# Kernel tuning notes

Measured on AMD Instinct MI355X. Metric: run time of the kernel, lower is better.

The kernel has to match this reference:

```python
import jax, jax.numpy as jnp
import numpy as np

B, P, C = 4, 2048, 1024
N_HEADS = 16
HEAD = C // N_HEADS


def setup_inputs() -> dict:
    key = jax.random.key(0)
    ks = jax.random.split(key, 9)
    s = C ** -0.5
    return {
        "x": jax.random.normal(ks[0], (B, P, C), dtype=jnp.float32),
        "Wq": jax.random.normal(ks[1], (C, C), dtype=jnp.float32) * s,
        "bq": jnp.zeros((C,), dtype=jnp.float32),
        "Wk": jax.random.normal(ks[2], (C, C), dtype=jnp.float32) * s,
        "bk": jnp.zeros((C,), dtype=jnp.float32),
        "Wv": jax.random.normal(ks[3], (C, C), dtype=jnp.float32) * s,
        "bv": jnp.zeros((C,), dtype=jnp.float32),
        "Wo": jax.random.normal(ks[4], (C, C), dtype=jnp.float32) * s,
        "bo": jnp.zeros((C,), dtype=jnp.float32),
    }


def _attn(x, Wq, bq, Wk, bk, Wv, bv, Wo, bo):
    b, p, c = x.shape
    q = (x @ Wq + bq).reshape(b, p, N_HEADS, HEAD).transpose(0, 2, 1, 3)
    k = (x @ Wk + bk).reshape(b, p, N_HEADS, HEAD).transpose(0, 2, 1, 3)
    v = (x @ Wv + bv).reshape(b, p, N_HEADS, HEAD).transpose(0, 2, 1, 3)
    # scores: [B, H, P, P]
    w = jnp.einsum('bhqd,bhkd->bhqk', q, k) * (HEAD ** -0.5)
    w = jax.nn.softmax(w, axis=-1)
    y = jnp.einsum('bhqk,bhkd->bhqd', w, v)
    y = y.transpose(0, 2, 1, 3).reshape(b, p, c)
    return y @ Wo + bo


def reference(x, Wq, bq, Wk, bk, Wv, bv, Wo, bo):
    return _attn(x, Wq, bq, Wk, bk, Wv, bv, Wo, bo)
```

## Files before the change

kernel.cpp:

```cpp
#include <hip/hip_runtime.h>

#define B_DIM 4
#define P_DIM 2048
#define C_DIM 1024
#define H_CNT 16
#define D_HEAD 64
#define M_DIM 8192
#define K_DIM 1024

typedef __attribute__((ext_vector_type(4))) float  f32x4;
typedef __attribute__((ext_vector_type(8))) __bf16 bf16x8;
typedef __attribute__((ext_vector_type(4))) __bf16 bf16x4;
typedef __attribute__((ext_vector_type(4))) short  s16x4;
typedef __attribute__((ext_vector_type(8))) short  s16x8;

static __device__ __forceinline__ short f2bf(float f) {
    unsigned u = __float_as_uint(f);
    u += 0x7fff + ((u >> 16) & 1);
    return (short)(u >> 16);
}

#define GLDS16(src, dst) __builtin_amdgcn_global_load_lds( \
    (__attribute__((address_space(1))) void*)(void*)(src), \
    (__attribute__((address_space(3))) void*)(void*)(dst), 16, 0, 0)

__global__ __launch_bounds__(256) void cvt_f32_bf16(const float* __restrict__ in,
                                                    short* __restrict__ out) {
    size_t i = ((size_t)blockIdx.x * 256 + threadIdx.x) * 4;
    f32x4 v = *(const f32x4*)(in + i);
    s16x4 o;
    o[0] = f2bf(v[0]); o[1] = f2bf(v[1]); o[2] = f2bf(v[2]); o[3] = f2bf(v[3]);
    *(s16x4*)(out + i) = o;
}

__global__ __launch_bounds__(256) void wtrans_all(const float* __restrict__ W0,
                                                  const float* __restrict__ W1,
                                                  const float* __restrict__ W2,
                                                  const float* __restrict__ W3,
                                                  short* __restrict__ WT) {
    __shared__ float t[32][33];
    const int z = blockIdx.z;
    const float* W = z == 0 ? W0 : z == 1 ? W1 : z == 2 ? W2 : W3;
    short* dst = WT + (size_t)z * C_DIM * C_DIM;
    const int k0 = blockIdx.y * 32, n0 = blockIdx.x * 32;
    const int tx = threadIdx.x & 31, ty = threadIdx.x >> 5;
#pragma unroll
    for (int j = 0; j < 4; ++j)
        t[ty + j * 8][tx] = W[(size_t)(k0 + ty + j * 8) * C_DIM + n0 + tx];
    __syncthreads();
#pragma unroll
    for (int j = 0; j < 4; ++j)
        dst[(size_t)(n0 + ty + j * 8) * C_DIM + k0 + tx] = f2bf(t[tx][ty + j * 8]);
}

template<int MODE>
__global__ __launch_bounds__(256) void gemm_bt(const short* __restrict__ A,
                                               const short* __restrict__ BT,
                                               const float* __restrict__ bias,
                                               const float* __restrict__ bias2,
                                               void* __restrict__ outp,
                                               int gx) {
    const int h = blockIdx.y * gx + blockIdx.x;
    const int cpx = (gx << 6) >> 3;
    const int lid = (h & 7) * cpx + (h >> 3);
    const int m0 = (lid / gx) * 128;
    const int n0 = (lid % gx) * 128;

    __shared__ __align__(16) short lA[128 * 32];
    __shared__ __align__(16) short lB[128 * 32];
    const int tid = threadIdx.x;
    const int lane = tid & 63;
    const int w = tid >> 6;
    const int wr = (w >> 1) * 64;
    const int wc = (w & 1) * 64;
    const int li = lane & 15, g = lane >> 4;

    f32x4 acc[4][4] = {};

    const int r0s = tid >> 2, r1s = (tid + 256) >> 2;
    const int c0 = (tid & 3) ^ ((r0s >> 1) & 3);
    const int c1 = (tid & 3) ^ ((r1s >> 1) & 3);
    const short* a0 = A + (size_t)(m0 + r0s) * K_DIM + c0 * 8;
    const short* a1 = A + (size_t)(m0 + r1s) * K_DIM + c1 * 8;
    const short* b0 = BT + (size_t)(n0 + r0s) * K_DIM + c0 * 8;
    const short* b1 = BT + (size_t)(n0 + r1s) * K_DIM + c1 * 8;
    short* lA0 = lA + w * 512;  short* lA1 = lA + 2048 + w * 512;
    short* lB0 = lB + w * 512;  short* lB1 = lB + 2048 + w * 512;

    int aoff[4], boff[4];
#pragma unroll
    for (int i = 0; i < 4; ++i) {
        int ra = wr + i * 16 + li;  int pa = g ^ ((ra >> 1) & 3);
        aoff[i] = ra * 32 + pa * 8;
        int rb = wc + i * 16 + li;  int pb = g ^ ((rb >> 1) & 3);
        boff[i] = rb * 32 + pb * 8;
    }

    for (int k0 = 0; k0 < K_DIM; k0 += 32) {
        __syncthreads();
        GLDS16(a0 + k0, lA0);
        GLDS16(a1 + k0, lA1);
        GLDS16(b0 + k0, lB0);
        GLDS16(b1 + k0, lB1);
        __syncthreads();
        bf16x8 af[4], bfr[4];
#pragma unroll
        for (int i = 0; i < 4; ++i) {
            af[i]  = *(const bf16x8*)&lA[aoff[i]];
            bfr[i] = *(const bf16x8*)&lB[boff[i]];
        }
#pragma unroll
        for (int i = 0; i < 4; ++i)
#pragma unroll
            for (int j = 0; j < 4; ++j) {
                if (MODE == 2)
                    acc[i][j] = __builtin_amdgcn_mfma_f32_16x16x32_bf16(
                        af[i], bfr[j], acc[i][j], 0, 0, 0);
                else
                    acc[i][j] = __builtin_amdgcn_mfma_f32_16x16x32_bf16(
                        bfr[j], af[i], acc[i][j], 0, 0, 0);
            }
    }

    if (MODE == 0) {
#pragma unroll
        for (int j = 0; j < 4; ++j) {
            const int nb = n0 + wc + j * 16 + 4 * g;
            const float* bp = nb < 1024 ? bias : bias2;
            const float sc = nb < 1024 ? 0.125f : 1.0f;
            const f32x4 bb = *(const f32x4*)&bp[nb & 1023];
            const int hI = (nb >> 6) & 15, d = nb & 63;
            short* base = (short*)outp + (size_t)(nb >> 10) * M_DIM * C_DIM;
#pragma unroll
            for (int i = 0; i < 4; ++i) {
                const int m = m0 + wr + i * 16 + li;
                const int bI = m >> 11, p = m & 2047;
                s16x4 v4;
#pragma unroll
                for (int r = 0; r < 4; ++r) v4[r] = f2bf((acc[i][j][r] + bb[r]) * sc);
                *(s16x4*)&base[(((size_t)bI * H_CNT + hI) * P_DIM + p) * D_HEAD + d] = v4;
            }
        }
    } else if (MODE == 1) {
#pragma unroll
        for (int j = 0; j < 4; ++j) {
            const int nb = n0 + wc + j * 16 + 4 * g;
            const f32x4 bb = *(const f32x4*)&bias[nb];
#pragma unroll
            for (int i = 0; i < 4; ++i) {
                const int m = m0 + wr + i * 16 + li;
                f32x4 v;
#pragma unroll
                for (int r = 0; r < 4; ++r) v[r] = acc[i][j][r] + bb[r];
                *(f32x4*)&((float*)outp)[(size_t)m * C_DIM + nb] = v;
            }
        }
    } else {
#pragma unroll
        for (int j = 0; j < 4; ++j) {
            const int nn = n0 + wc + j * 16 + li;
            const float bb = bias[nn];
            const int hI = nn >> 6, d = nn & 63;
#pragma unroll
            for (int i = 0; i < 4; ++i) {
                const int pbse = m0 + wr + i * 16 + 4 * g;
                const int bI = pbse >> 11, p = pbse & 2047;
                s16x4 v4;
#pragma unroll
                for (int r = 0; r < 4; ++r) v4[r] = f2bf(acc[i][j][r] + bb);
                *(s16x4*)&((short*)outp)[(((size_t)bI * H_CNT + hI) * D_HEAD + d) * P_DIM + p] = v4;
            }
        }
    }
}

__global__ __launch_bounds__(256, 4) void attn_fwd(const short* __restrict__ Q,
                                                   const short* __restrict__ Kb,
                                                   const short* __restrict__ VT,
                                                   short* __restrict__ Y) {
    const int flat = blockIdx.y * 16 + blockIdx.x;
    const int xcd = flat & 7, rr = flat >> 3;
    const int bh = xcd + 8 * (rr >> 4);
    const int qx = rr & 15;

    const int b = bh >> 4, h = bh & 15;
    const int tid = threadIdx.x;
    const int w = tid >> 6, lane = tid & 63;
    const int li = lane & 15, g = lane >> 4;
    const int x7 = li & 7;
    const int q0 = qx * 128 + w * 32;
    const short* Qh = Q + (size_t)bh * P_DIM * D_HEAD;
    const short* Kh = Kb + (size_t)bh * P_DIM * D_HEAD;
    const short* Vh = VT + (size_t)bh * D_HEAD * P_DIM;

    __shared__ __align__(16) short lK[64 * 64];
    __shared__ __align__(16) short lV[64 * 64];
    __shared__ __align__(16) short pb[4][32 * 64];
    short* pw = pb[w];

    bf16x8 qf[2][2];
#pragma unroll
    for (int qt = 0; qt < 2; ++qt)
#pragma unroll
        for (int c = 0; c < 2; ++c)
            qf[qt][c] = *(const bf16x8*)&Qh[(size_t)(q0 + qt * 16 + li) * D_HEAD + c * 32 + g * 8];

    f32x4 o[2][4] = {};
    float ps[2] = {};

    const int t1 = tid + 256;
    const int r0 = tid >> 3, u0 = (tid & 7) ^ (r0 & 7);
    const int r1 = t1 >> 3,  u1 = (t1 & 7) ^ (r1 & 7);
    const short* ks0 = Kh + r0 * D_HEAD + u0 * 8;
    const short* ks1 = Kh + r1 * D_HEAD + u1 * 8;
    const short* vs0 = Vh + r0 * P_DIM + u0 * 8;
    const short* vs1 = Vh + r1 * P_DIM + u1 * 8;
    short* dk0 = lK + tid * 8;  short* dk1 = lK + t1 * 8;
    short* dv0 = lV + tid * 8;  short* dv1 = lV + t1 * 8;

    const int pwrow0 = li * 64;
    const int wsw = x7 << 1;

    for (int k0 = 0; k0 < P_DIM; k0 += 64) {
        __syncthreads();
        GLDS16(ks0 + (size_t)k0 * D_HEAD, dk0);
        GLDS16(ks1 + (size_t)k0 * D_HEAD, dk1);
        GLDS16(vs0 + k0, dv0);
        GLDS16(vs1 + k0, dv1);
        __syncthreads();

        bf16x8 kf[4][2];
#pragma unroll
        for (int kt = 0; kt < 4; ++kt) {
            const int rbase = (kt * 16 + li) * 64;
            kf[kt][0] = *(const bf16x8*)&lK[rbase + ((0 + g) ^ x7) * 8];
            kf[kt][1] = *(const bf16x8*)&lK[rbase + ((4 + g) ^ x7) * 8];
        }

#pragma unroll
        for (int qt = 0; qt < 2; ++qt) {
            f32x4 s[4] = {};
#pragma unroll
            for (int kt = 0; kt < 4; ++kt) {
                s[kt] = __builtin_amdgcn_mfma_f32_16x16x32_bf16(kf[kt][0], qf[qt][0], s[kt], 0, 0, 0);
                s[kt] = __builtin_amdgcn_mfma_f32_16x16x32_bf16(kf[kt][1], qf[qt][1], s[kt], 0, 0, 0);
            }
            const int rowb = pwrow0 + qt * 16 * 64;
#pragma unroll
            for (int kt = 0; kt < 4; ++kt) {
                bf16x4 pv4;
#pragma unroll
                for (int r = 0; r < 4; ++r) {
                    float e = __expf(s[kt][r]);
                    ps[qt] += e;
                    pv4[r] = (__bf16)e;
                }
                const int j = (kt * 4 + g) ^ wsw;
                *(bf16x4*)&pw[rowb + j * 4] = pv4;
            }
        }
        __builtin_amdgcn_sched_barrier(0);
        asm volatile("s_waitcnt lgkmcnt(0)" ::: "memory");
        __builtin_amdgcn_sched_barrier(0);
#pragma unroll
        for (int kc = 0; kc < 2; ++kc) {
            bf16x8 pf[2];
#pragma unroll
            for (int qt = 0; qt < 2; ++qt) {
                const int j = (8 * kc + 2 * g) ^ wsw;
                pf[qt] = *(const bf16x8*)&pw[(qt * 16 + li) * 64 + j * 4];
            }
#pragma unroll
            for (int dt = 0; dt < 4; ++dt) {
                bf16x8 vf = *(const bf16x8*)&lV[(dt * 16 + li) * 64 + ((kc * 4 + g) ^ x7) * 8];
                o[0][dt] = __builtin_amdgcn_mfma_f32_16x16x32_bf16(pf[0], vf, o[0][dt], 0, 0, 0);
                o[1][dt] = __builtin_amdgcn_mfma_f32_16x16x32_bf16(pf[1], vf, o[1][dt], 0, 0, 0);
            }
        }
    }

#pragma unroll
    for (int qt = 0; qt < 2; ++qt) {
        float v = ps[qt];
        v += __shfl_xor(v, 16);
        v += __shfl_xor(v, 32);
#pragma unroll
        for (int r = 0; r < 4; ++r) {
            const float inv = 1.0f / __shfl(v, 4 * g + r);
            const int p = q0 + qt * 16 + 4 * g + r;
            short* yrow = Y + ((size_t)b * P_DIM + p) * C_DIM + h * D_HEAD;
#pragma unroll
            for (int dt = 0; dt < 4; ++dt)
                yrow[dt * 16 + li] = f2bf(o[qt][dt][r] * inv);
        }
    }
}

extern "C" void kernel_launch(void* const* d_in, const int* in_sizes, int n_in,
                              void* d_out, int out_size, void* d_ws, size_t ws_size,
                              hipStream_t stream) {
    (void)in_sizes; (void)n_in; (void)out_size; (void)ws_size;
    const float* x  = (const float*)d_in[0];
    const float* Wq = (const float*)d_in[1];
    const float* bq = (const float*)d_in[2];
    const float* Wk = (const float*)d_in[3];
    const float* bk = (const float*)d_in[4];
    const float* Wv = (const float*)d_in[5];
    const float* bv = (const float*)d_in[6];
    const float* Wo = (const float*)d_in[7];
    const float* bo = (const float*)d_in[8];

    short* ws  = (short*)d_ws;
    short* xb  = ws;
    short* wqt = xb  + (size_t)M_DIM * C_DIM;
    short* wvt = wqt + 2 * (size_t)C_DIM * C_DIM;
    short* wot = wqt + 3 * (size_t)C_DIM * C_DIM;
    short* qd  = wot + (size_t)C_DIM * C_DIM;
    short* kd  = qd  + (size_t)M_DIM * C_DIM;
    short* vtd = kd  + (size_t)M_DIM * C_DIM;
    short* yd  = vtd + (size_t)M_DIM * C_DIM;

    cvt_f32_bf16<<<dim3(M_DIM * C_DIM / 1024), 256, 0, stream>>>(x, xb);
    wtrans_all<<<dim3(32, 32, 4), 256, 0, stream>>>(Wq, Wk, Wv, Wo, wqt);
    gemm_bt<0><<<dim3(16, 64), 256, 0, stream>>>(xb, wqt, bq, bk, (void*)qd, 16);
    gemm_bt<2><<<dim3(8, 64), 256, 0, stream>>>(xb, wvt, bv, nullptr, (void*)vtd, 8);
    attn_fwd<<<dim3(16, 64), 256, 0, stream>>>(qd, kd, vtd, yd);
    gemm_bt<1><<<dim3(8, 64), 256, 0, stream>>>(yd, wot, bo, nullptr, d_out, 8);
}
```

Before: 202.1 us.

## Add dedicated 256x256-tile double-buffered QK projection GEMM kernel

```diff
diff --git a/kernel.cpp b/kernel.cpp
--- a/kernel.cpp
+++ b/kernel.cpp
@@ -51,6 +51,129 @@
 #pragma unroll
     for (int j = 0; j < 4; ++j)
         dst[(size_t)(n0 + ty + j * 8) * C_DIM + k0 + tx] = f2bf(t[tx][ty + j * 8]);
+}
+
+__global__ __launch_bounds__(512, 2) void gemm_qk8(const short* __restrict__ A,
+                                                   const short* __restrict__ BT,
+                                                   const float* __restrict__ bias,
+                                                   const float* __restrict__ bias2,
+                                                   short* __restrict__ outp) {
+    __shared__ __align__(16) short lA[2][256 * 64];
+    __shared__ __align__(16) short lB[2][256 * 64];
+    const int tid = threadIdx.x;
+    const int lane = tid & 63;
+    const int w = tid >> 6;
+    const int wm = w >> 2, wn = w & 3;
+    const int li = lane & 15, g = lane >> 4;
+
+    const int flat = blockIdx.y * 8 + blockIdx.x;
+    const int lid = (flat & 7) * 32 + (flat >> 3);
+    const int m0 = (lid >> 3) * 256;
+    const int n0 = (lid & 7) * 256;
+
+    const int e0 = tid, e1 = tid + 512;
+    const int r0 = e0 >> 3, lu0 = (e0 & 7) ^ (r0 & 7);
+    const int r1 = e1 >> 3, lu1 = (e1 & 7) ^ (r1 & 7);
+    const short* aS0 = A + (size_t)(m0 + r0) * K_DIM + lu0 * 8;
+    const short* aS1 = A + (size_t)(m0 + r1) * K_DIM + lu1 * 8;
+    const short* bS0 = BT + (size_t)(n0 + r0) * K_DIM + lu0 * 8;
+    const short* bS1 = BT + (size_t)(n0 + r1) * K_DIM + lu1 * 8;
+    const int dA0 = e0 * 8, dA1 = e1 * 8;
+
+#define STAGE_A8(buf, hh, kt) do { \
+    GLDS16(aS0 + (size_t)(hh) * 128 * K_DIM + (kt) * 64, &lA[buf][(hh) * 8192 + dA0]); \
+    GLDS16(aS1 + (size_t)(hh) * 128 * K_DIM + (kt) * 64, &lA[buf][(hh) * 8192 + dA1]); } while (0)
+#define STAGE_B8(buf, hh, kt) do { \
+    GLDS16(bS0 + (size_t)(hh) * 128 * K_DIM + (kt) * 64, &lB[buf][(hh) * 8192 + dB0]); \
+    GLDS16(bS1 + (size_t)(hh) * 128 * K_DIM + (kt) * 64, &lB[buf][(hh) * 8192 + dB1]); } while (0)
+    const int dB0 = dA0, dB1 = dA1;
+
+    int aoff[8][2], boff[4][2];
+#pragma unroll
+    for (int mrep = 0; mrep < 8; ++mrep) {
+        const int row = wm * 128 + mrep * 16 + li;
+#pragma unroll
+        for (int ks = 0; ks < 2; ++ks)
+            aoff[mrep][ks] = row * 64 + (((ks * 4 + g) ^ (row & 7)) * 8);
+    }
+#pragma unroll
+    for (int nrep = 0; nrep < 4; ++nrep) {
+        const int row = wn * 64 + nrep * 16 + li;
+#pragma unroll
+        for (int ks = 0; ks < 2; ++ks)
+            boff[nrep][ks] = row * 64 + (((ks * 4 + g) ^ (row & 7)) * 8);
+    }
+
+    f32x4 acc[8][4] = {};
+
+    STAGE_A8(0, 0, 0); STAGE_A8(0, 1, 0);
+    STAGE_B8(0, 0, 0); STAGE_B8(0, 1, 0);
+    asm volatile("s_waitcnt vmcnt(0)" ::: "memory");
+    __builtin_amdgcn_s_barrier();
+
+    for (int t = 0; t < 16; ++t) {
+        const int buf = t & 1;
+        const short* LA = lA[buf];
+        const short* LB = lB[buf];
+        bf16x8 bf[4][2];
+#pragma unroll
+        for (int p = 0; p < 4; ++p) {
+            if (p == 0) {
+#pragma unroll
+                for (int nrep = 0; nrep < 4; ++nrep)
+#pragma unroll
+                    for (int ks = 0; ks < 2; ++ks)
+                        bf[nrep][ks] = *(const bf16x8*)&LB[boff[nrep][ks]];
+            }
+            bf16x8 af2[2][2];
+#pragma unroll
+            for (int i = 0; i < 2; ++i)
+#pragma unroll
+                for (int ks = 0; ks < 2; ++ks)
+                    af2[i][ks] = *(const bf16x8*)&LA[aoff[2 * p + i][ks]];
+            if (t < 15) {
+                if (p == 0)      STAGE_A8(buf ^ 1, 0, t + 1);
+                else if (p == 1) STAGE_A8(buf ^ 1, 1, t + 1);
+                else if (p == 2) STAGE_B8(buf ^ 1, 0, t + 1);
+                else             STAGE_B8(buf ^ 1, 1, t + 1);
+            }
+            __builtin_amdgcn_s_barrier();
+            __builtin_amdgcn_s_setprio(1);
+#pragma unroll
+            for (int ks = 0; ks < 2; ++ks)
+#pragma unroll
+                for (int i = 0; i < 2; ++i)
+#pragma unroll
+                    for (int j = 0; j < 4; ++j)
+                        acc[2 * p + i][j] = __builtin_amdgcn_mfma_f32_16x16x32_bf16(
+                            bf[j][ks], af2[i][ks], acc[2 * p + i][j], 0, 0, 0);
+            __builtin_amdgcn_s_setprio(0);
+            __builtin_amdgcn_s_barrier();
+        }
+        asm volatile("s_waitcnt vmcnt(0)" ::: "memory");
+        __builtin_amdgcn_s_barrier();
+    }
+
+#pragma unroll
+    for (int nrep = 0; nrep < 4; ++nrep) {
+        const int nb = n0 + wn * 64 + nrep * 16 + 4 * g;
+        const float* bp = nb < 1024 ? bias : bias2;
+        const float sc = nb < 1024 ? 0.125f : 1.0f;
+        const f32x4 bb = *(const f32x4*)&bp[nb & 1023];
+        const int hI = (nb >> 6) & 15, d = nb & 63;
+        short* base = outp + (size_t)(nb >> 10) * M_DIM * C_DIM;
+#pragma unroll
+        for (int mrep = 0; mrep < 8; ++mrep) {
+            const int m = m0 + wm * 128 + mrep * 16 + li;
+            const int bI = m >> 11, p = m & 2047;
+            s16x4 v4;
+#pragma unroll
+            for (int r = 0; r < 4; ++r) v4[r] = f2bf((acc[mrep][nrep][r] + bb[r]) * sc);
+            *(s16x4*)&base[(((size_t)bI * H_CNT + hI) * P_DIM + p) * D_HEAD + d] = v4;
+        }
+    }
+#undef STAGE_A8
+#undef STAGE_B8
 }
 
 template<int MODE>
@@ -122,26 +245,7 @@
             }
     }
 
-    if (MODE == 0) {
-#pragma unroll
-        for (int j = 0; j < 4; ++j) {
-            const int nb = n0 + wc + j * 16 + 4 * g;
-            const float* bp = nb < 1024 ? bias : bias2;
-            const float sc = nb < 1024 ? 0.125f : 1.0f;
-            const f32x4 bb = *(const f32x4*)&bp[nb & 1023];
-            const int hI = (nb >> 6) & 15, d = nb & 63;
-            short* base = (short*)outp + (size_t)(nb >> 10) * M_DIM * C_DIM;
-#pragma unroll
-            for (int i = 0; i < 4; ++i) {
-                const int m = m0 + wr + i * 16 + li;
-                const int bI = m >> 11, p = m & 2047;
-                s16x4 v4;
-#pragma unroll
-                for (int r = 0; r < 4; ++r) v4[r] = f2bf((acc[i][j][r] + bb[r]) * sc);
-                *(s16x4*)&base[(((size_t)bI * H_CNT + hI) * P_DIM + p) * D_HEAD + d] = v4;
-            }
-        }
-    } else if (MODE == 1) {
+    if (MODE == 1) {
 #pragma unroll
         for (int j = 0; j < 4; ++j) {
             const int nb = n0 + wc + j * 16 + 4 * g;
@@ -322,7 +426,7 @@
 
     cvt_f32_bf16<<<dim3(M_DIM * C_DIM / 1024), 256, 0, stream>>>(x, xb);
     wtrans_all<<<dim3(32, 32, 4), 256, 0, stream>>>(Wq, Wk, Wv, Wo, wqt);
-    gemm_bt<0><<<dim3(16, 64), 256, 0, stream>>>(xb, wqt, bq, bk, (void*)qd, 16);
+    gemm_qk8<<<dim3(8, 32), 512, 0, stream>>>(xb, wqt, bq, bk, qd);
     gemm_bt<2><<<dim3(8, 64), 256, 0, stream>>>(xb, wvt, bv, nullptr, (void*)vtd, 8);
     attn_fwd<<<dim3(16, 64), 256, 0, stream>>>(qd, kd, vtd, yd);
     gemm_bt<1><<<dim3(8, 64), 256, 0, stream>>>(yd, wot, bo, nullptr, d_out, 8);
```

Measured after the change: 194.9 us. 3.6% less time.
